# Kernel tuning notes

Hardware: AMD Instinct MI355X
Metric: run time of the kernel (lower is better)

The kernel has to match this reference:

```python
import jax, jax.numpy as jnp
import numpy as np

D_MODEL = 1024
BATCH = 16
SEQ = 1024
RATIO = 2.0 / 3.0  # layer_idx=2, n_layers=4
THRESH = 0.5


def _layer_norm(x, gamma, beta, eps=1e-5):
    mu = jnp.mean(x, axis=-1, keepdims=True)
    var = jnp.var(x, axis=-1, keepdims=True)
    return (x - mu) * jax.lax.rsqrt(var + eps) * gamma + beta


def _ternary(x):
    # FixedThresholdTernarySpike(threshold=0.5): sign(x) if |x|>0.5 else 0
    return jnp.where(x > THRESH, 1.0, jnp.where(x < -THRESH, -1.0, 0.0)).astype(x.dtype)


def setup_inputs() -> dict:
    key = jax.random.key(0)
    ks = jax.random.split(key, 10)
    scale = 0.1 / np.sqrt(D_MODEL)
    x = jax.random.normal(ks[0], (BATCH, SEQ, D_MODEL), dtype=jnp.float32)
    S0 = jnp.zeros((BATCH, D_MODEL), dtype=jnp.float32)
    mix_init = 1.0 - RATIO
    return {
        "x": x,
        "S0": S0,
        "ln_gamma": jnp.ones((D_MODEL,), jnp.float32),
        "ln_beta": jnp.zeros((D_MODEL,), jnp.float32),
        "time_mix_k": jnp.full((D_MODEL,), mix_init, jnp.float32) + 0.02 * jax.random.normal(ks[1], (D_MODEL,)),
        "time_mix_v": jnp.full((D_MODEL,), mix_init, jnp.float32) + 0.02 * jax.random.normal(ks[2], (D_MODEL,)),
        "time_mix_r": jnp.full((D_MODEL,), mix_init, jnp.float32) + 0.02 * jax.random.normal(ks[3], (D_MODEL,)),
        "decay_weight": jnp.full((D_MODEL,), -0.5, jnp.float32) + 0.02 * jax.random.normal(ks[4], (D_MODEL,)),
        "Wk": scale * jax.random.normal(ks[5], (D_MODEL, D_MODEL), jnp.float32),
        "Wv": scale * jax.random.normal(ks[6], (D_MODEL, D_MODEL), jnp.float32),
        "Wr": scale * jax.random.normal(ks[7], (D_MODEL, D_MODEL), jnp.float32),
        "Wo": scale * jax.random.normal(ks[8], (D_MODEL, D_MODEL), jnp.float32),
    }


def reference(x, S0, ln_gamma, ln_beta, time_mix_k, time_mix_v, time_mix_r,
              decay_weight, Wk, Wv, Wr, Wo):
    # x: (B, T, D)
    x_norm = _layer_norm(x, ln_gamma, ln_beta)                       # LN applied to every step
    # prev_x at t is LN(x[t-1]); at t=0 it is zeros (module uses zeros_like, not LN of zeros)
    prev_norm = jnp.concatenate([jnp.zeros_like(x_norm[:, :1]), x_norm[:, :-1]], axis=1)

    xk = x_norm * time_mix_k + prev_norm * (1.0 - time_mix_k)
    xv = x_norm * time_mix_v + prev_norm * (1.0 - time_mix_v)
    xr = x_norm * time_mix_r + prev_norm * (1.0 - time_mix_r)

    k = _ternary(jnp.einsum('btd,ed->bte', xk, Wk))                  # ternary spikes
    v = _ternary(jnp.einsum('btd,ed->bte', xv, Wv))
    r = jax.nn.sigmoid(jnp.einsum('btd,ed->bte', xr, Wr))

    decay = jax.nn.sigmoid(decay_weight)                             # (D,)
    kv = k * v                                                       # (B, T, D)

    def step(S, kv_t):                                               # S: (B, D)
        S_new = decay * S + kv_t
        return S_new, S_new

    S_final, S_all = jax.lax.scan(step, S0, jnp.swapaxes(kv, 0, 1))  # S_all: (T, B, D)
    S_all = jnp.swapaxes(S_all, 0, 1)                                # (B, T, D)

    out = x + r * jnp.einsum('btd,ed->bte', S_all, Wo)
    return out, S_final
```

## Files before the change

### kernel.cpp

```cpp
#include <hip/hip_runtime.h>
#include <hip/hip_bf16.h>
#include <math.h>

#define D_MODEL 1024
#define SEQ 1024
#define BATCH 16
#define NROWS (BATCH * SEQ)
#define KT8 8

typedef float f32x4 __attribute__((ext_vector_type(4)));
typedef int   i32x4 __attribute__((ext_vector_type(4)));
typedef int   i32x8 __attribute__((ext_vector_type(8)));
typedef __hip_bfloat16 bf16;
typedef unsigned char u8;

__device__ __forceinline__ float bf2f(bf16 v) { return __bfloat162float(v); }
__device__ __forceinline__ bf16 f2bf(float v) { return __float2bfloat16(v); }

__device__ __forceinline__ void gload_lds16(const u8* g, u8* l) {
    __builtin_amdgcn_global_load_lds(
        (const __attribute__((address_space(1))) void*)g,
        (__attribute__((address_space(3))) void*)l, 16, 0, 0);
}

__device__ __forceinline__ int pk_fp8x4(float a, float b, float c, float d) {
    int r = __builtin_amdgcn_cvt_pk_fp8_f32(a, b, 0, false);
    r = __builtin_amdgcn_cvt_pk_fp8_f32(c, d, r, true);
    return r;
}

__device__ __forceinline__ void tile_coords128(int lin, int& m0, int& n0) {
    const int xcd = lin & 7;
    const int loc = lin >> 3;
    m0 = (xcd * 16 + (loc & 15)) * 128;
    n0 = (loc >> 4) * 128;
}

__global__ void conv_w4_kernel(const float* __restrict__ s0, const float* __restrict__ s1,
                               const float* __restrict__ s2, const float* __restrict__ s3,
                               u8* __restrict__ dst) {
    const float* srcs[4] = {s0, s1, s2, s3};
    const float* src = srcs[blockIdx.y];
    int* d = reinterpret_cast<int*>(dst + (size_t)blockIdx.y * (D_MODEL * D_MODEL));
    int i = blockIdx.x * blockDim.x + threadIdx.x;
    const int stride = gridDim.x * blockDim.x;
    for (; i < (D_MODEL * D_MODEL) / 4; i += stride) {
        float4 f = reinterpret_cast<const float4*>(src)[i];
        d[i] = pk_fp8x4(f.x, f.y, f.z, f.w);
    }
}

__global__ __launch_bounds__(256) void lnmix_kernel(
    const float* __restrict__ x, const float* __restrict__ gamma, const float* __restrict__ beta,
    const float* __restrict__ tmk, const float* __restrict__ tmv, const float* __restrict__ tmr,
    u8* __restrict__ xk, u8* __restrict__ xv, u8* __restrict__ xr)
{
    const int wave = threadIdx.x >> 6, lane = threadIdx.x & 63;
    const int lb = (blockIdx.x & 7) * (gridDim.x >> 3) + (blockIdx.x >> 3);
    const int row = lb * 4 + wave;
    const int t = row & (SEQ - 1);
    const size_t base = (size_t)row * D_MODEL;

    float4 vc[4], vp[4];
    float sc = 0.f, sc2 = 0.f, sp = 0.f, sp2 = 0.f;
#pragma unroll
    for (int c = 0; c < 4; c++) {
        const int d = lane * 4 + c * 256;
        vc[c] = *reinterpret_cast<const float4*>(x + base + d);
        if (t == 0) { vp[c] = make_float4(0.f, 0.f, 0.f, 0.f); }
        else        { vp[c] = *reinterpret_cast<const float4*>(x + base - D_MODEL + d); }
        sc  += vc[c].x + vc[c].y + vc[c].z + vc[c].w;
        sc2 += vc[c].x * vc[c].x + vc[c].y * vc[c].y + vc[c].z * vc[c].z + vc[c].w * vc[c].w;
        sp  += vp[c].x + vp[c].y + vp[c].z + vp[c].w;
        sp2 += vp[c].x * vp[c].x + vp[c].y * vp[c].y + vp[c].z * vp[c].z + vp[c].w * vp[c].w;
    }
#pragma unroll
    for (int off = 1; off < 64; off <<= 1) {
        sc  += __shfl_xor(sc, off);
        sc2 += __shfl_xor(sc2, off);
        sp  += __shfl_xor(sp, off);
        sp2 += __shfl_xor(sp2, off);
    }
    const float muc = sc * (1.0f / D_MODEL);
    const float rc  = rsqrtf(sc2 * (1.0f / D_MODEL) - muc * muc + 1e-5f);
    const float mup = sp * (1.0f / D_MODEL);
    const float rp  = rsqrtf(sp2 * (1.0f / D_MODEL) - mup * mup + 1e-5f);

#pragma unroll
    for (int c = 0; c < 4; c++) {
        const int d = lane * 4 + c * 256;
        float4 g  = *reinterpret_cast<const float4*>(gamma + d);
        float4 b  = *reinterpret_cast<const float4*>(beta + d);
        float4 mk = *reinterpret_cast<const float4*>(tmk + d);
        float4 mv = *reinterpret_cast<const float4*>(tmv + d);
        float4 mr = *reinterpret_cast<const float4*>(tmr + d);
        float cn[4], pn[4];
        cn[0] = (vc[c].x - muc) * rc * g.x + b.x;
        cn[1] = (vc[c].y - muc) * rc * g.y + b.y;
        cn[2] = (vc[c].z - muc) * rc * g.z + b.z;
        cn[3] = (vc[c].w - muc) * rc * g.w + b.w;
        if (t == 0) { pn[0] = pn[1] = pn[2] = pn[3] = 0.f; }
        else {
            pn[0] = (vp[c].x - mup) * rp * g.x + b.x;
            pn[1] = (vp[c].y - mup) * rp * g.y + b.y;
            pn[2] = (vp[c].z - mup) * rp * g.z + b.z;
            pn[3] = (vp[c].w - mup) * rp * g.w + b.w;
        }
        const float mkv[4] = {mk.x, mk.y, mk.z, mk.w};
        const float mvv[4] = {mv.x, mv.y, mv.z, mv.w};
        const float mrv[4] = {mr.x, mr.y, mr.z, mr.w};
        float ok[4], ov[4], orr[4];
#pragma unroll
        for (int e = 0; e < 4; e++) {
            ok[e]  = mkv[e] * cn[e] + (1.0f - mkv[e]) * pn[e];
            ov[e]  = mvv[e] * cn[e] + (1.0f - mvv[e]) * pn[e];
            orr[e] = mrv[e] * cn[e] + (1.0f - mrv[e]) * pn[e];
        }
        *reinterpret_cast<int*>(xk + base + d) = pk_fp8x4(ok[0], ok[1], ok[2], ok[3]);
        *reinterpret_cast<int*>(xv + base + d) = pk_fp8x4(ov[0], ov[1], ov[2], ov[3]);
        *reinterpret_cast<int*>(xr + base + d) = pk_fp8x4(orr[0], orr[1], orr[2], orr[3]);
    }
}

__device__ __forceinline__ void gemm128_fp8_core(
    const u8* __restrict__ A, const u8* __restrict__ W,
    u8* __restrict__ As, u8* __restrict__ Bs,
    int m0, int n0, f32x4 (&acc)[4][4])
{
    const int tid  = threadIdx.x;
    const int wave = tid >> 6, lane = tid & 63;
    const int wm = wave >> 1, wn = wave & 1;
    const int mf = lane & 15, quad = lane >> 4;
    const int srow = tid >> 3;
    const int u  = (tid & 7) ^ (srow & 7);
    const int sw = (((u & 3) << 1) | (u >> 2)) * 16;

    const u8* Ag = A + (size_t)(m0 + srow) * D_MODEL + sw;
    const u8* Bg = W + (size_t)(n0 + srow) * D_MODEL + sw;

    const int swz0 = ((quad)     ^ (mf & 7)) * 16;
    const int swz1 = ((4 + quad) ^ (mf & 7)) * 16;
    const u8* aB0 = As + (wm * 64 + mf) * 128 + swz0;
    const u8* aB1 = As + (wm * 64 + mf) * 128 + swz1;
    const u8* bB0 = Bs + (wn * 64 + mf) * 128 + swz0;
    const u8* bB1 = Bs + (wn * 64 + mf) * 128 + swz1;

#pragma unroll 1
    for (int kt = 0; kt < KT8; ++kt) {
        __syncthreads();
#pragma unroll
        for (int g = 0; g < 4; ++g) {
            gload_lds16(Ag + (size_t)g * 32 * D_MODEL + kt * 128, As + g * 4096 + wave * 1024);
            gload_lds16(Bg + (size_t)g * 32 * D_MODEL + kt * 128, Bs + g * 4096 + wave * 1024);
        }
        __syncthreads();

        i32x8 af[4], bf[4];
#pragma unroll
        for (int i = 0; i < 4; ++i) {
            i32x4 lo = *reinterpret_cast<const i32x4*>(aB0 + i * 2048);
            i32x4 hi = *reinterpret_cast<const i32x4*>(aB1 + i * 2048);
            af[i] = __builtin_shufflevector(lo, hi, 0, 1, 2, 3, 4, 5, 6, 7);
        }
#pragma unroll
        for (int j = 0; j < 4; ++j) {
            i32x4 lo = *reinterpret_cast<const i32x4*>(bB0 + j * 2048);
            i32x4 hi = *reinterpret_cast<const i32x4*>(bB1 + j * 2048);
            bf[j] = __builtin_shufflevector(lo, hi, 0, 1, 2, 3, 4, 5, 6, 7);
        }
#pragma unroll
        for (int i = 0; i < 4; ++i)
#pragma unroll
            for (int j = 0; j < 4; ++j)
                acc[i][j] = __builtin_amdgcn_mfma_scale_f32_16x16x128_f8f6f4(
                    af[i], bf[j], acc[i][j], 0, 0, 0, 127, 0, 127);
    }
}

__global__ __launch_bounds__(256) void gemm128_kv(
    const u8* __restrict__ A0, const u8* __restrict__ A1,
    const u8* __restrict__ W0, const u8* __restrict__ W1,
    char* __restrict__ O0, char* __restrict__ O1)
{
    const u8* A = blockIdx.y ? A1 : A0;
    const u8* W = blockIdx.y ? W1 : W0;
    char* O     = blockIdx.y ? O1 : O0;

    __shared__ __align__(16) u8 As[16384];
    __shared__ __align__(16) u8 Bs[16384];
    int m0, n0;
    tile_coords128(blockIdx.x, m0, n0);

    f32x4 acc[4][4] = {};
    gemm128_fp8_core(A, W, As, Bs, m0, n0, acc);

    const int lane = threadIdx.x & 63, wave = threadIdx.x >> 6;
    const int wm = wave >> 1, wn = wave & 1;
    const int mf = lane & 15, quad = lane >> 4;
#pragma unroll
    for (int i = 0; i < 4; ++i)
#pragma unroll
        for (int j = 0; j < 4; ++j)
#pragma unroll
            for (int e = 0; e < 4; ++e) {
                const int row = m0 + wm * 64 + i * 16 + quad * 4 + e;
                const int col = n0 + wn * 64 + j * 16 + mf;
                const float v = acc[i][j][e];
                O[(size_t)row * D_MODEL + col] = (v > 0.5f) ? 1 : ((v < -0.5f) ? -1 : 0);
            }
}

__global__ __launch_bounds__(512) void scan_kernel(
    const char* __restrict__ K8, const char* __restrict__ V8,
    const float* __restrict__ dw, const float* __restrict__ S0,
    u8* __restrict__ sall, float* __restrict__ sfinal)
{
    __shared__ unsigned int kvp[8][8][64];
    __shared__ float Lf[8][64];
    __shared__ float P[8][64];

    const int bid = blockIdx.x;
    const int db  = bid & 15, b = bid >> 4;
    const int ch  = threadIdx.x & 63;
    const int q   = threadIdx.x >> 6;
    const int d   = db * 64 + ch;

    const float dec = 1.0f / (1.0f + __expf(-dw[d]));
    float c128 = dec;
#pragma unroll
    for (int i = 0; i < 7; i++) c128 *= c128;

    const size_t base = ((size_t)b * SEQ + q * 128) * D_MODEL + d;

    float S = 0.f;
    size_t idx = base;
    unsigned int w = 0;
    for (int t = 0; t < 128; t += 4, idx += 4 * D_MODEL) {
        const int k0 = K8[idx];
        const int v0 = V8[idx];
        const int k1 = K8[idx + 1 * D_MODEL];
        const int v1 = V8[idx + 1 * D_MODEL];
        const int k2 = K8[idx + 2 * D_MODEL];
        const int v2 = V8[idx + 2 * D_MODEL];
        const int k3 = K8[idx + 3 * D_MODEL];
        const int v3 = V8[idx + 3 * D_MODEL];
        const int p0 = k0 * v0, p1 = k1 * v1, p2 = k2 * v2, p3 = k3 * v3;
        S = dec * S + (float)p0;
        S = dec * S + (float)p1;
        S = dec * S + (float)p2;
        S = dec * S + (float)p3;
        const int sh = 2 * (t & 15);
        w |= ((unsigned int)(p0 + 1) << sh) | ((unsigned int)(p1 + 1) << (sh + 2)) |
             ((unsigned int)(p2 + 1) << (sh + 4)) | ((unsigned int)(p3 + 1) << (sh + 6));
        if ((t & 15) == 12) { kvp[q][t >> 4][ch] = w; w = 0; }
    }

    Lf[q][ch] = S;
    __syncthreads();
    if (q == 0) {
        float p = S0[b * D_MODEL + d];
        P[0][ch] = p;
#pragma unroll
        for (int j = 1; j < 8; ++j) {
            p = Lf[j - 1][ch] + c128 * p;
            P[j][ch] = p;
        }
        p = Lf[7][ch] + c128 * p;
        sfinal[b * D_MODEL + d] = p;
    }
    __syncthreads();

    float Sv = P[q][ch];
    idx = base;
    for (int t16 = 0; t16 < 8; ++t16) {
        const unsigned int pw = kvp[q][t16][ch];
#pragma unroll
        for (int j = 0; j < 16; ++j, idx += D_MODEL) {
            const float p = (float)((int)((pw >> (2 * j)) & 3) - 1);
            Sv = dec * Sv + p;
            const int enc = __builtin_amdgcn_cvt_pk_fp8_f32(Sv, 0.f, 0, false);
            sall[idx] = (u8)(enc & 255);
        }
    }
}

__global__ __launch_bounds__(256, 2) void gemm128_outR(
    const u8* __restrict__ XR, const u8* __restrict__ Wr,
    const u8* __restrict__ SA, const u8* __restrict__ Wo,
    const float* __restrict__ x, float* __restrict__ out)
{
    __shared__ __align__(16) u8 As[16384];
    __shared__ __align__(16) u8 Bs[16384];
    int m0, n0;
    tile_coords128(blockIdx.x, m0, n0);

    f32x4 accR[4][4] = {};
    gemm128_fp8_core(XR, Wr, As, Bs, m0, n0, accR);
#pragma unroll
    for (int i = 0; i < 4; ++i)
#pragma unroll
        for (int j = 0; j < 4; ++j)
#pragma unroll
            for (int e = 0; e < 4; ++e)
                accR[i][j][e] = 1.0f / (1.0f + __expf(-accR[i][j][e]));

    f32x4 acc[4][4] = {};
    gemm128_fp8_core(SA, Wo, As, Bs, m0, n0, acc);

    const int lane = threadIdx.x & 63, wave = threadIdx.x >> 6;
    const int wm = wave >> 1, wn = wave & 1;
    const int mf = lane & 15, quad = lane >> 4;
#pragma unroll
    for (int i = 0; i < 4; ++i)
#pragma unroll
        for (int j = 0; j < 4; ++j)
#pragma unroll
            for (int e = 0; e < 4; ++e) {
                const int row = m0 + wm * 64 + i * 16 + quad * 4 + e;
                const int col = n0 + wn * 64 + j * 16 + mf;
                const size_t o = (size_t)row * D_MODEL + col;
                out[o] = x[o] + accR[i][j][e] * acc[i][j][e];
            }
}

extern "C" void kernel_launch(void* const* d_in, const int* in_sizes, int n_in,
                              void* d_out, int out_size, void* d_ws, size_t ws_size,
                              hipStream_t stream) {
    const float* x     = (const float*)d_in[0];
    const float* S0    = (const float*)d_in[1];
    const float* gamma = (const float*)d_in[2];
    const float* beta  = (const float*)d_in[3];
    const float* tmk   = (const float*)d_in[4];
    const float* tmv   = (const float*)d_in[5];
    const float* tmr   = (const float*)d_in[6];
    const float* dw    = (const float*)d_in[7];
    const float* Wk    = (const float*)d_in[8];
    const float* Wv    = (const float*)d_in[9];
    const float* Wr    = (const float*)d_in[10];
    const float* Wo    = (const float*)d_in[11];
    float* out = (float*)d_out;

    const int WN = D_MODEL * D_MODEL;
    const size_t MATN = (size_t)NROWS * D_MODEL;

    u8* ws   = (u8*)d_ws;
    u8* Wk8  = ws;
    u8* Wv8  = Wk8 + WN;
    u8* Wr8  = Wv8 + WN;
    u8* Wo8  = Wr8 + WN;
    u8* XK8  = Wo8 + WN;
    u8* XV8  = XK8 + MATN;
    u8* XR8  = XV8 + MATN;
    char* Kt8 = (char*)(XR8 + MATN);
    char* Vt8 = Kt8 + MATN;
    u8* SA8  = (u8*)(Vt8 + MATN);

    conv_w4_kernel<<<dim3(256, 4), 256, 0, stream>>>(Wk, Wv, Wr, Wo, ws);

    lnmix_kernel<<<NROWS / 4, 256, 0, stream>>>(x, gamma, beta, tmk, tmv, tmr, XK8, XV8, XR8);

    gemm128_kv<<<dim3(1024, 2), 256, 0, stream>>>(XK8, XV8, Wk8, Wv8, Kt8, Vt8);

    scan_kernel<<<256, 512, 0, stream>>>(Kt8, Vt8, dw, S0, SA8, out + MATN);

    gemm128_outR<<<1024, 256, 0, stream>>>(XR8, Wr8, SA8, Wo8, x, out);
}
```

Measured before the change: 270.2 us.

## Interleave paired FP8 GEMMs in one K-loop sharing barriers

Replaces the single-GEMM core with a dual version that loads A/B tiles for two independent GEMMs per K step into a 64KB LDS buffer and issues both MFMA groups between the same barriers. The K/V projection launch is halved to one grid where each block computes both outputs, and the R/Wo kernel runs its two GEMMs interleaved rather than back to back. The aim is to halve the number of barrier/load phases and give more independent MFMA work per sync. The cost is doubled LDS (64KB per block) and two accumulator sets, which raises register pressure and may cut occupancy.

```diff
diff --git a/kernel.cpp b/kernel.cpp
--- a/kernel.cpp
+++ b/kernel.cpp
@@ -122,10 +122,11 @@
     }
 }
 
-__device__ __forceinline__ void gemm128_fp8_core(
-    const u8* __restrict__ A, const u8* __restrict__ W,
-    u8* __restrict__ As, u8* __restrict__ Bs,
-    int m0, int n0, f32x4 (&acc)[4][4])
+__device__ __forceinline__ void gemm128_fp8_dual(
+    const u8* __restrict__ A0, const u8* __restrict__ W0,
+    const u8* __restrict__ A1, const u8* __restrict__ W1,
+    u8* __restrict__ lds,
+    int m0, int n0, f32x4 (&acc0)[4][4], f32x4 (&acc1)[4][4])
 {
     const int tid  = threadIdx.x;
     const int wave = tid >> 6, lane = tid & 63;
@@ -135,64 +136,86 @@
     const int u  = (tid & 7) ^ (srow & 7);
     const int sw = (((u & 3) << 1) | (u >> 2)) * 16;
 
-    const u8* Ag = A + (size_t)(m0 + srow) * D_MODEL + sw;
-    const u8* Bg = W + (size_t)(n0 + srow) * D_MODEL + sw;
+    const u8* A0g = A0 + (size_t)(m0 + srow) * D_MODEL + sw;
+    const u8* B0g = W0 + (size_t)(n0 + srow) * D_MODEL + sw;
+    const u8* A1g = A1 + (size_t)(m0 + srow) * D_MODEL + sw;
+    const u8* B1g = W1 + (size_t)(n0 + srow) * D_MODEL + sw;
+
+    u8* As0 = lds;
+    u8* Bs0 = lds + 16384;
+    u8* As1 = lds + 32768;
+    u8* Bs1 = lds + 49152;
 
     const int swz0 = ((quad)     ^ (mf & 7)) * 16;
     const int swz1 = ((4 + quad) ^ (mf & 7)) * 16;
-    const u8* aB0 = As + (wm * 64 + mf) * 128 + swz0;
-    const u8* aB1 = As + (wm * 64 + mf) * 128 + swz1;
-    const u8* bB0 = Bs + (wn * 64 + mf) * 128 + swz0;
-    const u8* bB1 = Bs + (wn * 64 + mf) * 128 + swz1;
+    const int aRow = (wm * 64 + mf) * 128;
+    const int bRow = (wn * 64 + mf) * 128;
 
 #pragma unroll 1
     for (int kt = 0; kt < KT8; ++kt) {
         __syncthreads();
 #pragma unroll
         for (int g = 0; g < 4; ++g) {
-            gload_lds16(Ag + (size_t)g * 32 * D_MODEL + kt * 128, As + g * 4096 + wave * 1024);
-            gload_lds16(Bg + (size_t)g * 32 * D_MODEL + kt * 128, Bs + g * 4096 + wave * 1024);
+            const size_t go = (size_t)g * 32 * D_MODEL + kt * 128;
+            const int lo = g * 4096 + wave * 1024;
+            gload_lds16(A0g + go, As0 + lo);
+            gload_lds16(B0g + go, Bs0 + lo);
+            gload_lds16(A1g + go, As1 + lo);
+            gload_lds16(B1g + go, Bs1 + lo);
         }
         __syncthreads();
 
         i32x8 af[4], bf[4];
 #pragma unroll
         for (int i = 0; i < 4; ++i) {
-            i32x4 lo = *reinterpret_cast<const i32x4*>(aB0 + i * 2048);
-            i32x4 hi = *reinterpret_cast<const i32x4*>(aB1 + i * 2048);
+            i32x4 lo = *reinterpret_cast<const i32x4*>(As0 + aRow + i * 2048 + swz0);
+            i32x4 hi = *reinterpret_cast<const i32x4*>(As0 + aRow + i * 2048 + swz1);
             af[i] = __builtin_shufflevector(lo, hi, 0, 1, 2, 3, 4, 5, 6, 7);
         }
 #pragma unroll
         for (int j = 0; j < 4; ++j) {
-            i32x4 lo = *reinterpret_cast<const i32x4*>(bB0 + j * 2048);
-            i32x4 hi = *reinterpret_cast<const i32x4*>(bB1 + j * 2048);
+            i32x4 lo = *reinterpret_cast<const i32x4*>(Bs0 + bRow + j * 2048 + swz0);
+            i32x4 hi = *reinterpret_cast<const i32x4*>(Bs0 + bRow + j * 2048 + swz1);
             bf[j] = __builtin_shufflevector(lo, hi, 0, 1, 2, 3, 4, 5, 6, 7);
         }
 #pragma unroll
         for (int i = 0; i < 4; ++i)
 #pragma unroll
             for (int j = 0; j < 4; ++j)
-                acc[i][j] = __builtin_amdgcn_mfma_scale_f32_16x16x128_f8f6f4(
-                    af[i], bf[j], acc[i][j], 0, 0, 0, 127, 0, 127);
-    }
-}
-
-__global__ __launch_bounds__(256) void gemm128_kv(
-    const u8* __restrict__ A0, const u8* __restrict__ A1,
-    const u8* __restrict__ W0, const u8* __restrict__ W1,
-    char* __restrict__ O0, char* __restrict__ O1)
-{
-    const u8* A = blockIdx.y ? A1 : A0;
-    const u8* W = blockIdx.y ? W1 : W0;
-    char* O     = blockIdx.y ? O1 : O0;
-
-    __shared__ __align__(16) u8 As[16384];
-    __shared__ __align__(16) u8 Bs[16384];
+                acc0[i][j] = __builtin_amdgcn_mfma_scale_f32_16x16x128_f8f6f4(
+                    af[i], bf[j], acc0[i][j], 0, 0, 0, 127, 0, 127);
+#pragma unroll
+        for (int i = 0; i < 4; ++i) {
+            i32x4 lo = *reinterpret_cast<const i32x4*>(As1 + aRow + i * 2048 + swz0);
+            i32x4 hi = *reinterpret_cast<const i32x4*>(As1 + aRow + i * 2048 + swz1);
+            af[i] = __builtin_shufflevector(lo, hi, 0, 1, 2, 3, 4, 5, 6, 7);
+        }
+#pragma unroll
+        for (int j = 0; j < 4; ++j) {
+            i32x4 lo = *reinterpret_cast<const i32x4*>(Bs1 + bRow + j * 2048 + swz0);
+            i32x4 hi = *reinterpret_cast<const i32x4*>(Bs1 + bRow + j * 2048 + swz1);
+            bf[j] = __builtin_shufflevector(lo, hi, 0, 1, 2, 3, 4, 5, 6, 7);
+        }
+#pragma unroll
+        for (int i = 0; i < 4; ++i)
+#pragma unroll
+            for (int j = 0; j < 4; ++j)
+                acc1[i][j] = __builtin_amdgcn_mfma_scale_f32_16x16x128_f8f6f4(
+                    af[i], bf[j], acc1[i][j], 0, 0, 0, 127, 0, 127);
+    }
+}
+
+__global__ __launch_bounds__(256, 2) void gemm128_kv(
+    const u8* __restrict__ XK, const u8* __restrict__ Wk,
+    const u8* __restrict__ XV, const u8* __restrict__ Wv,
+    char* __restrict__ OK, char* __restrict__ OV)
+{
+    __shared__ __align__(16) u8 lds[65536];
     int m0, n0;
     tile_coords128(blockIdx.x, m0, n0);
 
-    f32x4 acc[4][4] = {};
-    gemm128_fp8_core(A, W, As, Bs, m0, n0, acc);
+    f32x4 acc0[4][4] = {}, acc1[4][4] = {};
+    gemm128_fp8_dual(XK, Wk, XV, Wv, lds, m0, n0, acc0, acc1);
 
     const int lane = threadIdx.x & 63, wave = threadIdx.x >> 6;
     const int wm = wave >> 1, wn = wave & 1;
@@ -205,8 +228,11 @@
             for (int e = 0; e < 4; ++e) {
                 const int row = m0 + wm * 64 + i * 16 + quad * 4 + e;
                 const int col = n0 + wn * 64 + j * 16 + mf;
-                const float v = acc[i][j][e];
-                O[(size_t)row * D_MODEL + col] = (v > 0.5f) ? 1 : ((v < -0.5f) ? -1 : 0);
+                const size_t o = (size_t)row * D_MODEL + col;
+                const float k = acc0[i][j][e];
+                const float v = acc1[i][j][e];
+                OK[o] = (k > 0.5f) ? 1 : ((k < -0.5f) ? -1 : 0);
+                OV[o] = (v > 0.5f) ? 1 : ((v < -0.5f) ? -1 : 0);
             }
 }
 
@@ -289,23 +315,12 @@
     const u8* __restrict__ SA, const u8* __restrict__ Wo,
     const float* __restrict__ x, float* __restrict__ out)
 {
-    __shared__ __align__(16) u8 As[16384];
-    __shared__ __align__(16) u8 Bs[16384];
+    __shared__ __align__(16) u8 lds[65536];
     int m0, n0;
     tile_coords128(blockIdx.x, m0, n0);
 
-    f32x4 accR[4][4] = {};
-    gemm128_fp8_core(XR, Wr, As, Bs, m0, n0, accR);
-#pragma unroll
-    for (int i = 0; i < 4; ++i)
-#pragma unroll
-        for (int j = 0; j < 4; ++j)
-#pragma unroll
-            for (int e = 0; e < 4; ++e)
-                accR[i][j][e] = 1.0f / (1.0f + __expf(-accR[i][j][e]));
-
-    f32x4 acc[4][4] = {};
-    gemm128_fp8_core(SA, Wo, As, Bs, m0, n0, acc);
+    f32x4 accR[4][4] = {}, acc[4][4] = {};
+    gemm128_fp8_dual(XR, Wr, SA, Wo, lds, m0, n0, accR, acc);
 
     const int lane = threadIdx.x & 63, wave = threadIdx.x >> 6;
     const int wm = wave >> 1, wn = wave & 1;
@@ -319,7 +334,8 @@
                 const int row = m0 + wm * 64 + i * 16 + quad * 4 + e;
                 const int col = n0 + wn * 64 + j * 16 + mf;
                 const size_t o = (size_t)row * D_MODEL + col;
-                out[o] = x[o] + accR[i][j][e] * acc[i][j][e];
+                const float r = 1.0f / (1.0f + __expf(-accR[i][j][e]));
+                out[o] = x[o] + r * acc[i][j][e];
             }
 }
 
@@ -359,7 +375,7 @@
 
     lnmix_kernel<<<NROWS / 4, 256, 0, stream>>>(x, gamma, beta, tmk, tmv, tmr, XK8, XV8, XR8);
 
-    gemm128_kv<<<dim3(1024, 2), 256, 0, stream>>>(XK8, XV8, Wk8, Wv8, Kt8, Vt8);
+    gemm128_kv<<<1024, 256, 0, stream>>>(XK8, Wk8, XV8, Wv8, Kt8, Vt8);
 
     scan_kernel<<<256, 512, 0, stream>>>(Kt8, Vt8, dw, S0, SA8, out + MATN);
 
```

Result: no change. 268.6 us (-0.6%).
